# Optimization experiments

Hardware: AMD Instinct MI355X
Metric: run time of the kernel (lower is better)

## Reference

```python
import jax, jax.numpy as jnp
import numpy as np

B, H, N, C = 32768, 1024, 4, 1000
BN_EPS = 1e-5        # weighted batch norm epsilon
IG_EPS = 1e-30       # info-gain log epsilon (as in CIGN repo)
TEMPERATURE = 1.0    # routing temperature
BALANCE = 2.0        # information gain balance coefficient


def setup_inputs() -> dict:
    key = jax.random.key(0)
    k = jax.random.split(key, 4)
    return {
        "ig_mask": jax.random.randint(k[0], (B,), 0, 2, dtype=jnp.int32),
        "h_net": jax.random.normal(k[1], (B, H), dtype=jnp.float32),
        "labels": jax.random.randint(k[2], (B,), 0, C, dtype=jnp.int32),
        "gamma": jnp.ones((H,), jnp.float32),
        "beta": jnp.zeros((H,), jnp.float32),
        "W": jax.random.normal(k[3], (H, N), dtype=jnp.float32) * 0.03,
        "b": jnp.zeros((N,), jnp.float32),
    }


def _weighted_batch_norm(x, mask_f, gamma, beta):
    # mask-weighted batch statistics; normalization applied to ALL samples
    w = mask_f[:, None]                       # [B,1]
    wsum = jnp.sum(mask_f)
    mean = jnp.sum(w * x, axis=0) / wsum      # [H]
    var = jnp.sum(w * (x - mean) ** 2, axis=0) / wsum
    return gamma * (x - mean) * jax.lax.rsqrt(var + BN_EPS) + beta


def _info_gain(activations, labels, mask_f):
    sample_count = jnp.sum(mask_f)
    pv = mask_f / sample_count                              # [B]
    p_n_given_x = jax.nn.softmax(activations / TEMPERATURE, axis=1)  # [B,N]
    onehot = jax.nn.one_hot(labels, C, dtype=activations.dtype)      # [B,C]
    # joint p(c,n) = sum_b pv[b] * onehot[b,c] * p_n_given_x[b,n]
    p_cn = jnp.einsum('b,bc,bn->cn', pv, onehot, p_n_given_x)        # [C,N]
    p_n = jnp.sum(p_cn, axis=0)                                      # [N]
    p_c = jnp.sum(p_cn, axis=1)                                      # [C]
    kv = p_cn * (jnp.log(p_cn + IG_EPS)
                 - jnp.log(p_c + IG_EPS)[:, None]
                 - BALANCE * jnp.log(p_n + IG_EPS)[None, :])
    return -jnp.sum(kv)


def reference(ig_mask, h_net, labels, gamma, beta, W, b):
    mask_f = ig_mask.astype(jnp.float32)
    h_normed = _weighted_batch_norm(h_net, mask_f, gamma, beta)      # [B,H]
    activations = h_normed @ W + b                                   # [B,N]
    ig_value = _info_gain(activations, labels, mask_f)               # scalar
    routing = jax.nn.one_hot(jnp.argmax(activations, axis=1), N, dtype=jnp.int32)
    out_routing = jnp.logical_and(routing.astype(bool),
                                  ig_mask[:, None].astype(bool)).astype(jnp.int32)
    return h_normed, ig_value, out_routing
```

## Files before the change

### kernel.cpp

```cpp
#include <hip/hip_runtime.h>
#include <cstddef>

#define B_SZ 32768
#define H_SZ 1024
#define N_SZ 4
#define C_SZ 1000
#define ROW_BLOCKS 2048
#define ROWS_PER_BLOCK 16

#define PART_SUM   0
#define PART_SQ    (PART_SUM + ROW_BLOCKS*H_SZ)
#define WSUM_PART  (PART_SQ  + ROW_BLOCKS*H_SZ)
#define A_OFF      (WSUM_PART + ROW_BLOCKS)
#define C_OFF      (A_OFF + H_SZ)
#define SCAL_OFF   (C_OFF + H_SZ)
#define PCN_OFF    (SCAL_OFF + 8)

#define OUT_IG  ((size_t)B_SZ * H_SZ)
#define OUT_R   (OUT_IG + 1)

__global__ void __launch_bounds__(256) k_colsum(const float* __restrict__ h,
                                                const int* __restrict__ mask,
                                                float* __restrict__ ws) {
    const int rb   = blockIdx.x;
    const int t    = threadIdx.x;
    const int row0 = rb * ROWS_PER_BLOCK;
    const int col  = t * 4;

    if (rb < 500 && t < 8) ws[PCN_OFF + rb * 8 + t] = 0.f;

    float4 sA = make_float4(0.f, 0.f, 0.f, 0.f);
    float4 qA = make_float4(0.f, 0.f, 0.f, 0.f);
    float4 sB = make_float4(0.f, 0.f, 0.f, 0.f);
    float4 qB = make_float4(0.f, 0.f, 0.f, 0.f);
    int mc = 0;

    const float* p = h + (size_t)row0 * H_SZ + col;
#pragma unroll
    for (int r = 0; r < ROWS_PER_BLOCK; r += 2) {
        const int   ma = mask[row0 + r];
        const int   mb = mask[row0 + r + 1];
        const float wa = (float)ma;
        const float wb = (float)mb;
        const float4 xa = *(const float4*)(p);
        const float4 xb = *(const float4*)(p + H_SZ);
        mc += ma + mb;

        float tx;
        tx = wa * xa.x; sA.x += tx; qA.x = fmaf(tx, xa.x, qA.x);
        tx = wa * xa.y; sA.y += tx; qA.y = fmaf(tx, xa.y, qA.y);
        tx = wa * xa.z; sA.z += tx; qA.z = fmaf(tx, xa.z, qA.z);
        tx = wa * xa.w; sA.w += tx; qA.w = fmaf(tx, xa.w, qA.w);

        tx = wb * xb.x; sB.x += tx; qB.x = fmaf(tx, xb.x, qB.x);
        tx = wb * xb.y; sB.y += tx; qB.y = fmaf(tx, xb.y, qB.y);
        tx = wb * xb.z; sB.z += tx; qB.z = fmaf(tx, xb.z, qB.z);
        tx = wb * xb.w; sB.w += tx; qB.w = fmaf(tx, xb.w, qB.w);

        p += 2 * H_SZ;
    }
    sA.x += sB.x; sA.y += sB.y; sA.z += sB.z; sA.w += sB.w;
    qA.x += qB.x; qA.y += qB.y; qA.z += qB.z; qA.w += qB.w;

    *(float4*)(ws + PART_SUM + (size_t)rb * H_SZ + col) = sA;
    *(float4*)(ws + PART_SQ  + (size_t)rb * H_SZ + col) = qA;
    if (t == 0) ws[WSUM_PART + rb] = (float)mc;
}

__global__ void __launch_bounds__(256) k_colfinal(const float* __restrict__ gamma,
                                                  const float* __restrict__ beta,
                                                  float* __restrict__ ws) {
    __shared__ float red[256];
    __shared__ float sh_s[32][9];
    __shared__ float sh_q[32][9];
    const int t = threadIdx.x;

    float w = 0.f;
#pragma unroll
    for (int i = 0; i < ROW_BLOCKS / 256; ++i) w += ws[WSUM_PART + i * 256 + t];
    red[t] = w;
    __syncthreads();
    for (int sft = 128; sft > 0; sft >>= 1) {
        if (t < sft) red[t] += red[t + sft];
        __syncthreads();
    }
    const float wsum = red[0];

    const int c8    = t & 7;
    const int strip = t >> 3;
    const int col   = blockIdx.x * 8 + c8;

    float s = 0.f, q = 0.f;
    const int rb0 = strip * (ROW_BLOCKS / 32);
    for (int k = 0; k < ROW_BLOCKS / 32; ++k) {
        s += ws[PART_SUM + (size_t)(rb0 + k) * H_SZ + col];
        q += ws[PART_SQ  + (size_t)(rb0 + k) * H_SZ + col];
    }
    sh_s[strip][c8] = s;
    sh_q[strip][c8] = q;
    __syncthreads();

    if (t < 8) {
        float S = 0.f, Q = 0.f;
#pragma unroll
        for (int k = 0; k < 32; ++k) { S += sh_s[k][t]; Q += sh_q[k][t]; }
        const int hcol = blockIdx.x * 8 + t;
        const float inv_w = 1.0f / wsum;
        const float mean  = S * inv_w;
        float var = Q * inv_w - mean * mean;
        if (var < 0.f) var = 0.f;
        const float istd = rsqrtf(var + 1e-5f);
        const float a = gamma[hcol] * istd;
        const float c = beta[hcol] - mean * a;
        ws[A_OFF + hcol] = a;
        ws[C_OFF + hcol] = c;
        if (blockIdx.x == 0 && t == 0) ws[SCAL_OFF] = inv_w;
    }
}

__global__ void __launch_bounds__(256, 3) k_fused(const float* __restrict__ hin,
                                                  const int* __restrict__ mask,
                                                  const int* __restrict__ labels,
                                                  const float* __restrict__ W,
                                                  const float* __restrict__ bias,
                                                  const float* __restrict__ ws,
                                                  float* __restrict__ out,
                                                  float* __restrict__ pcn) {
    const int wid  = threadIdx.x >> 6;
    const int lane = threadIdx.x & 63;
    const int gw   = blockIdx.x * 4 + wid;
    const int row0 = gw * 4;

    float4 Wr[4][4];
    float4 a4[4], c4[4];
#pragma unroll
    for (int ch = 0; ch < 4; ++ch) {
        const int h = ch * 256 + lane * 4;
        a4[ch] = *(const float4*)(ws + A_OFF + h);
        c4[ch] = *(const float4*)(ws + C_OFF + h);
#pragma unroll
        for (int j = 0; j < 4; ++j)
            Wr[ch][j] = *(const float4*)(W + (size_t)(h + j) * 4);
    }
    const float inv_w = ws[SCAL_OFF];

    float4 accA, accB, accC, accD;

#define ROW_BODY(ACC, RIDX)                                                     \
    {                                                                           \
        const int row = row0 + (RIDX);                                          \
        const float* xr   = hin + (size_t)row * H_SZ;                           \
        float*       outr = out + (size_t)row * H_SZ;                           \
        ACC = make_float4(0.f, 0.f, 0.f, 0.f);                                  \
        _Pragma("unroll")                                                       \
        for (int ch = 0; ch < 4; ++ch) {                                        \
            const int h = ch * 256 + lane * 4;                                  \
            const float4 x = *(const float4*)(xr + h);                          \
            float4 hn;                                                          \
            hn.x = fmaf(x.x, a4[ch].x, c4[ch].x);                               \
            hn.y = fmaf(x.y, a4[ch].y, c4[ch].y);                               \
            hn.z = fmaf(x.z, a4[ch].z, c4[ch].z);                               \
            hn.w = fmaf(x.w, a4[ch].w, c4[ch].w);                               \
            *(float4*)(outr + h) = hn;                                          \
            ACC.x = fmaf(hn.x, Wr[ch][0].x, ACC.x);                             \
            ACC.y = fmaf(hn.x, Wr[ch][0].y, ACC.y);                             \
            ACC.z = fmaf(hn.x, Wr[ch][0].z, ACC.z);                             \
            ACC.w = fmaf(hn.x, Wr[ch][0].w, ACC.w);                             \
            ACC.x = fmaf(hn.y, Wr[ch][1].x, ACC.x);                             \
            ACC.y = fmaf(hn.y, Wr[ch][1].y, ACC.y);                             \
            ACC.z = fmaf(hn.y, Wr[ch][1].z, ACC.z);                             \
            ACC.w = fmaf(hn.y, Wr[ch][1].w, ACC.w);                             \
            ACC.x = fmaf(hn.z, Wr[ch][2].x, ACC.x);                             \
            ACC.y = fmaf(hn.z, Wr[ch][2].y, ACC.y);                             \
            ACC.z = fmaf(hn.z, Wr[ch][2].z, ACC.z);                             \
            ACC.w = fmaf(hn.z, Wr[ch][2].w, ACC.w);                             \
            ACC.x = fmaf(hn.w, Wr[ch][3].x, ACC.x);                             \
            ACC.y = fmaf(hn.w, Wr[ch][3].y, ACC.y);                             \
            ACC.z = fmaf(hn.w, Wr[ch][3].z, ACC.z);                             \
            ACC.w = fmaf(hn.w, Wr[ch][3].w, ACC.w);                             \
        }                                                                       \
    }

    ROW_BODY(accA, 0)
    ROW_BODY(accB, 1)
    ROW_BODY(accC, 2)
    ROW_BODY(accD, 3)
#undef ROW_BODY

#pragma unroll
    for (int off = 1; off < 64; off <<= 1) {
        accA.x += __shfl_xor(accA.x, off); accA.y += __shfl_xor(accA.y, off);
        accA.z += __shfl_xor(accA.z, off); accA.w += __shfl_xor(accA.w, off);
        accB.x += __shfl_xor(accB.x, off); accB.y += __shfl_xor(accB.y, off);
        accB.z += __shfl_xor(accB.z, off); accB.w += __shfl_xor(accB.w, off);
        accC.x += __shfl_xor(accC.x, off); accC.y += __shfl_xor(accC.y, off);
        accC.z += __shfl_xor(accC.z, off); accC.w += __shfl_xor(accC.w, off);
        accD.x += __shfl_xor(accD.x, off); accD.y += __shfl_xor(accD.y, off);
        accD.z += __shfl_xor(accD.z, off); accD.w += __shfl_xor(accD.w, off);
    }

    if (lane < 16) {
        const int r   = lane >> 2;
        const int n   = lane & 3;
        const int row = row0 + r;

        const float4 av = (r == 0) ? accA : (r == 1) ? accB : (r == 2) ? accC : accD;

        const float s0 = av.x + bias[0];
        const float s1 = av.y + bias[1];
        const float s2 = av.z + bias[2];
        const float s3 = av.w + bias[3];

        int amax = 0; float best = s0;
        if (s1 > best) { best = s1; amax = 1; }
        if (s2 > best) { best = s2; amax = 2; }
        if (s3 > best) { best = s3; amax = 3; }

        const float e0 = expf(s0 - best);
        const float e1 = expf(s1 - best);
        const float e2 = expf(s2 - best);
        const float e3 = expf(s3 - best);
        const float inv = 1.0f / (e0 + e1 + e2 + e3);

        const int m = mask[row];
        const float rv = (m && n == amax) ? 1.0f : 0.0f;
        out[OUT_R + (size_t)row * 4 + n] = rv;
        if (m) {
            const float en = (n == 0 ? e0 : n == 1 ? e1 : n == 2 ? e2 : e3);
            atomicAdd(&pcn[labels[row] * 4 + n], en * inv * inv_w);
        }
    }
}

__global__ void __launch_bounds__(256) k_ig(const float* __restrict__ pcn,
                                            float* __restrict__ out) {
    __shared__ float red[256];
    __shared__ float pn_sh[4];
    const int t = threadIdx.x;

    float pn[4] = {0.f, 0.f, 0.f, 0.f};
    for (int c = t; c < C_SZ; c += 256) {
        pn[0] += pcn[c * 4 + 0];
        pn[1] += pcn[c * 4 + 1];
        pn[2] += pcn[c * 4 + 2];
        pn[3] += pcn[c * 4 + 3];
    }
#pragma unroll
    for (int n = 0; n < 4; ++n) {
        red[t] = pn[n];
        __syncthreads();
        for (int sft = 128; sft > 0; sft >>= 1) {
            if (t < sft) red[t] += red[t + sft];
            __syncthreads();
        }
        if (t == 0) pn_sh[n] = red[0];
        __syncthreads();
    }

    const float l0 = 2.0f * logf(pn_sh[0] + 1e-30f);
    const float l1 = 2.0f * logf(pn_sh[1] + 1e-30f);
    const float l2 = 2.0f * logf(pn_sh[2] + 1e-30f);
    const float l3 = 2.0f * logf(pn_sh[3] + 1e-30f);

    float kv = 0.f;
    for (int c = t; c < C_SZ; c += 256) {
        const float v0 = pcn[c * 4 + 0];
        const float v1 = pcn[c * 4 + 1];
        const float v2 = pcn[c * 4 + 2];
        const float v3 = pcn[c * 4 + 3];
        const float pc  = v0 + v1 + v2 + v3;
        const float lpc = logf(pc + 1e-30f);
        kv += v0 * (logf(v0 + 1e-30f) - lpc - l0);
        kv += v1 * (logf(v1 + 1e-30f) - lpc - l1);
        kv += v2 * (logf(v2 + 1e-30f) - lpc - l2);
        kv += v3 * (logf(v3 + 1e-30f) - lpc - l3);
    }
    red[t] = kv;
    __syncthreads();
    for (int sft = 128; sft > 0; sft >>= 1) {
        if (t < sft) red[t] += red[t + sft];
        __syncthreads();
    }
    if (t == 0) out[OUT_IG] = -red[0];
}

extern "C" void kernel_launch(void* const* d_in, const int* in_sizes, int n_in,
                              void* d_out, int out_size, void* d_ws, size_t ws_size,
                              hipStream_t stream) {
    const int*   ig_mask = (const int*)d_in[0];
    const float* h_net   = (const float*)d_in[1];
    const int*   labels  = (const int*)d_in[2];
    const float* gamma   = (const float*)d_in[3];
    const float* beta    = (const float*)d_in[4];
    const float* W       = (const float*)d_in[5];
    const float* b       = (const float*)d_in[6];

    float* out = (float*)d_out;
    float* ws  = (float*)d_ws;

    k_colsum<<<ROW_BLOCKS, 256, 0, stream>>>(h_net, ig_mask, ws);
    k_colfinal<<<H_SZ / 8, 256, 0, stream>>>(gamma, beta, ws);
    k_fused<<<B_SZ / 16, 256, 0, stream>>>(h_net, ig_mask, labels, W, b, ws, out,
                                           ws + PCN_OFF);
    k_ig<<<1, 256, 0, stream>>>(ws + PCN_OFF, out);
}
```

Measured before the change: 93.75 us.

## Reverse colsum row order for cache reuse and widen colfinal to one column per block

The column-stats kernel now walks row blocks in reverse, so the rows read last are the first rows the fused kernel reads next, which is meant to leave them in the last-level cache. The finalize kernel now uses one block per column with a 256-way tree reduction of sum, square sum and mask weight, instead of 8 columns per block. The goal is more parallelism in the finalize step and fewer cache misses when the fused kernel starts. The trade-off is strided, uncoalesced reads of the partials in finalize (each thread reads one float per 4KB row) and a redundant mask-weight reduction in every block.

```diff
diff --git a/kernel.cpp b/kernel.cpp
--- a/kernel.cpp
+++ b/kernel.cpp
@@ -24,7 +24,7 @@
                                                 float* __restrict__ ws) {
     const int rb   = blockIdx.x;
     const int t    = threadIdx.x;
-    const int row0 = rb * ROWS_PER_BLOCK;
+    const int row0 = B_SZ - (rb + 1) * ROWS_PER_BLOCK;
     const int col  = t * 4;
 
     if (rb < 500 && t < 8) ws[PCN_OFF + rb * 8 + t] = 0.f;
@@ -70,51 +70,35 @@
 __global__ void __launch_bounds__(256) k_colfinal(const float* __restrict__ gamma,
                                                   const float* __restrict__ beta,
                                                   float* __restrict__ ws) {
-    __shared__ float red[256];
-    __shared__ float sh_s[32][9];
-    __shared__ float sh_q[32][9];
-    const int t = threadIdx.x;
-
-    float w = 0.f;
-#pragma unroll
-    for (int i = 0; i < ROW_BLOCKS / 256; ++i) w += ws[WSUM_PART + i * 256 + t];
-    red[t] = w;
+    __shared__ float rs[256], rq[256], rw[256];
+    const int t   = threadIdx.x;
+    const int col = blockIdx.x;
+
+    float s = 0.f, q = 0.f, w = 0.f;
+#pragma unroll
+    for (int k = 0; k < ROW_BLOCKS / 256; ++k) {
+        const int rb = t + k * 256;
+        s += ws[PART_SUM + (size_t)rb * H_SZ + col];
+        q += ws[PART_SQ  + (size_t)rb * H_SZ + col];
+        w += ws[WSUM_PART + rb];
+    }
+    rs[t] = s; rq[t] = q; rw[t] = w;
     __syncthreads();
     for (int sft = 128; sft > 0; sft >>= 1) {
-        if (t < sft) red[t] += red[t + sft];
-        __syncthreads();
-    }
-    const float wsum = red[0];
-
-    const int c8    = t & 7;
-    const int strip = t >> 3;
-    const int col   = blockIdx.x * 8 + c8;
-
-    float s = 0.f, q = 0.f;
-    const int rb0 = strip * (ROW_BLOCKS / 32);
-    for (int k = 0; k < ROW_BLOCKS / 32; ++k) {
-        s += ws[PART_SUM + (size_t)(rb0 + k) * H_SZ + col];
-        q += ws[PART_SQ  + (size_t)(rb0 + k) * H_SZ + col];
-    }
-    sh_s[strip][c8] = s;
-    sh_q[strip][c8] = q;
-    __syncthreads();
-
-    if (t < 8) {
-        float S = 0.f, Q = 0.f;
-#pragma unroll
-        for (int k = 0; k < 32; ++k) { S += sh_s[k][t]; Q += sh_q[k][t]; }
-        const int hcol = blockIdx.x * 8 + t;
+        if (t < sft) { rs[t] += rs[t+sft]; rq[t] += rq[t+sft]; rw[t] += rw[t+sft]; }
+        __syncthreads();
+    }
+    if (t == 0) {
+        const float wsum  = rw[0];
         const float inv_w = 1.0f / wsum;
-        const float mean  = S * inv_w;
-        float var = Q * inv_w - mean * mean;
+        const float mean  = rs[0] * inv_w;
+        float var = rq[0] * inv_w - mean * mean;
         if (var < 0.f) var = 0.f;
         const float istd = rsqrtf(var + 1e-5f);
-        const float a = gamma[hcol] * istd;
-        const float c = beta[hcol] - mean * a;
-        ws[A_OFF + hcol] = a;
-        ws[C_OFF + hcol] = c;
-        if (blockIdx.x == 0 && t == 0) ws[SCAL_OFF] = inv_w;
+        const float a = gamma[col] * istd;
+        ws[A_OFF + col] = a;
+        ws[C_OFF + col] = beta[col] - mean * a;
+        if (col == 0) ws[SCAL_OFF] = inv_w;
     }
 }
 
@@ -299,7 +283,7 @@
     float* ws  = (float*)d_ws;
 
     k_colsum<<<ROW_BLOCKS, 256, 0, stream>>>(h_net, ig_mask, ws);
-    k_colfinal<<<H_SZ / 8, 256, 0, stream>>>(gamma, beta, ws);
+    k_colfinal<<<H_SZ, 256, 0, stream>>>(gamma, beta, ws);
     k_fused<<<B_SZ / 16, 256, 0, stream>>>(h_net, ig_mask, labels, W, b, ws, out,
                                            ws + PCN_OFF);
     k_ig<<<1, 256, 0, stream>>>(ws + PCN_OFF, out);
```

After: 114.7 us. 1.22x slower.
